# Performance work log

Hardware: AMD Instinct MI355X
Metric: run time of the kernel (lower is better)

The kernel has to match this reference:

```python
import jax, jax.numpy as jnp
import numpy as np

GAMMA = 2.0
SMOOTH = 1e-08
ALPHA_SMOOTH = 0.1


def setup_inputs() -> dict:
    key = jax.random.key(0)
    k1, k2 = jax.random.split(key)
    N, C, H, W = 8, 16, 512, 512
    logits = jax.random.normal(k1, (N, C, H, W), dtype=jnp.float32)
    target = jax.random.randint(k2, (N, H, W), 0, C, dtype=jnp.int64)
    return {"logits": logits, "target": target}


def _adaptive_alpha(target, num_classes):
    # histogram of class counts (fixed size -> jit friendly)
    counts = jnp.zeros((num_classes,), jnp.float32).at[target.reshape(-1)].add(1.0)
    total = jnp.asarray(target.size, jnp.float32)
    freq = counts / total
    w = 1.0 / (freq + ALPHA_SMOOTH)
    present = counts > 0
    wsum = jnp.sum(jnp.where(present, w, 0.0))
    # absent classes keep alpha = 1.0, matching torch.unique-based assignment
    return jnp.where(present, w / wsum, 1.0)


def reference(logits, target):
    # logits: (N, C, H, W) float; target: (N, H, W) int
    C = logits.shape[1]
    alpha = _adaptive_alpha(target, C)  # (C,)
    p = jax.nn.softmax(logits, axis=1)
    # gather probability of true class: equivalent to the one-hot loop, since
    # focal_c is multiplied by t_c so only positions with target==c contribute,
    # where p_t == p_c.
    p_true = jnp.take_along_axis(p, target[:, None, :, :], axis=1)[:, 0]  # (N,H,W)
    focal = alpha[target] * (1.0 - p_true + SMOOTH) ** GAMMA * (-jnp.log(p_true + SMOOTH))
    num_positives = jnp.asarray(target.size, jnp.float32)  # one-hot sum
    return jnp.sum(focal) / (num_positives + SMOOTH)
```

## Files before the change

### kernel.cpp

```cpp
#include <hip/hip_runtime.h>

#define HWSZ   262144
#define NCLS   16
#define NPIX   2097152
#define NQ     524288
#define GRID   1024
#define BLOCK  256
#define NCOPY  16

__global__ __launch_bounds__(BLOCK) void focal_main(
    const float* __restrict__ logits,
    const int*   __restrict__ target,
    float*       __restrict__ pb,
    unsigned*    __restrict__ pc)
{
    __shared__ float    sbin[NCOPY][NCLS];
    __shared__ unsigned scnt[NCOPY][NCLS];
    for (int i = threadIdx.x; i < NCOPY * NCLS; i += BLOCK) {
        ((float*)sbin)[i]    = 0.0f;
        ((unsigned*)scnt)[i] = 0u;
    }
    __syncthreads();

    const int copy = threadIdx.x & (NCOPY - 1);

    for (int q = blockIdx.x * BLOCK + threadIdx.x; q < NQ; q += GRID * BLOCK) {
        const int n  = q >> 16;
        const int s4 = (q & 65535) << 2;
        const float* base = logits + (size_t)n * (NCLS * HWSZ) + s4;
        const int4 t4 = *(const int4*)(target + ((size_t)q << 2));

        float4 ssum = make_float4(0.f, 0.f, 0.f, 0.f);
        float4 et   = make_float4(0.f, 0.f, 0.f, 0.f);
#pragma unroll
        for (int c = 0; c < NCLS; ++c) {
            const float4 v = *(const float4*)(base + (size_t)c * HWSZ);
            float ex;
            ex = __expf(v.x); ssum.x += ex; et.x = (t4.x == c) ? ex : et.x;
            ex = __expf(v.y); ssum.y += ex; et.y = (t4.y == c) ? ex : et.y;
            ex = __expf(v.z); ssum.z += ex; et.z = (t4.z == c) ? ex : et.z;
            ex = __expf(v.w); ssum.w += ex; et.w = (t4.w == c) ? ex : et.w;
        }

        float p, b;
        p = et.x * __builtin_amdgcn_rcpf(ssum.x);
        b = 1.0f - p + 1e-8f; b = b * b * (-__logf(p + 1e-8f));
        atomicAdd(&sbin[copy][t4.x & 15], b);
        atomicAdd(&scnt[copy][t4.x & 15], 1u);

        p = et.y * __builtin_amdgcn_rcpf(ssum.y);
        b = 1.0f - p + 1e-8f; b = b * b * (-__logf(p + 1e-8f));
        atomicAdd(&sbin[copy][t4.y & 15], b);
        atomicAdd(&scnt[copy][t4.y & 15], 1u);

        p = et.z * __builtin_amdgcn_rcpf(ssum.z);
        b = 1.0f - p + 1e-8f; b = b * b * (-__logf(p + 1e-8f));
        atomicAdd(&sbin[copy][t4.z & 15], b);
        atomicAdd(&scnt[copy][t4.z & 15], 1u);

        p = et.w * __builtin_amdgcn_rcpf(ssum.w);
        b = 1.0f - p + 1e-8f; b = b * b * (-__logf(p + 1e-8f));
        atomicAdd(&sbin[copy][t4.w & 15], b);
        atomicAdd(&scnt[copy][t4.w & 15], 1u);
    }
    __syncthreads();

    if (threadIdx.x < NCLS) {
        float    s  = 0.0f;
        unsigned n2 = 0u;
        for (int k = 0; k < NCOPY; ++k) {
            s  += sbin[k][threadIdx.x];
            n2 += scnt[k][threadIdx.x];
        }
        pb[threadIdx.x * GRID + blockIdx.x] = s;
        pc[threadIdx.x * GRID + blockIdx.x] = n2;
    }
}

__global__ __launch_bounds__(256) void focal_finalize(
    const float*    __restrict__ pb,
    const unsigned* __restrict__ pc,
    float*          __restrict__ out)
{
    __shared__ double   sb[NCLS][16];
    __shared__ unsigned sn[NCLS][16];
    const int c   = threadIdx.x >> 4;
    const int seg = threadIdx.x & 15;

    const float4* pbv = (const float4*)(pb + c * GRID + seg * 64);
    const uint4*  pcv = (const uint4*)(pc + c * GRID + seg * 64);
    double   s = 0.0;
    unsigned n = 0u;
#pragma unroll
    for (int i = 0; i < 16; ++i) {
        const float4 f = pbv[i];
        s += (double)f.x + (double)f.y + (double)f.z + (double)f.w;
        const uint4 u = pcv[i];
        n += u.x + u.y + u.z + u.w;
    }
    sb[c][seg] = s;
    sn[c][seg] = n;
    __syncthreads();

    if (threadIdx.x < NCLS) {
        double   S   = 0.0;
        unsigned cnt = 0u;
        for (int k = 0; k < 16; ++k) { S += sb[threadIdx.x][k]; cnt += sn[threadIdx.x][k]; }
        sb[threadIdx.x][0] = S;
        sn[threadIdx.x][0] = cnt;
    }
    __syncthreads();

    if (threadIdx.x == 0) {
        const double total = (double)NPIX;
        double w[NCLS];
        double wsum = 0.0;
        for (int k = 0; k < NCLS; ++k) {
            const double freq = (double)sn[k][0] / total;
            w[k] = 1.0 / (freq + 0.1);
            if (sn[k][0] > 0u) wsum += w[k];
        }
        double loss = 0.0;
        for (int k = 0; k < NCLS; ++k) {
            const double alpha = (sn[k][0] > 0u) ? (w[k] / wsum) : 1.0;
            loss += alpha * sb[k][0];
        }
        out[0] = (float)(loss / (total + 1e-8));
    }
}

extern "C" void kernel_launch(void* const* d_in, const int* in_sizes, int n_in,
                              void* d_out, int out_size, void* d_ws, size_t ws_size,
                              hipStream_t stream)
{
    const float* logits = (const float*)d_in[0];
    const int*   target = (const int*)d_in[1];

    float*    pb = (float*)d_ws;
    unsigned* pc = (unsigned*)((char*)d_ws + (size_t)NCLS * GRID * sizeof(float));

    focal_main<<<GRID, BLOCK, 0, stream>>>(logits, target, pb, pc);
    focal_finalize<<<1, 256, 0, stream>>>(pb, pc, (float*)d_out);
}
```

Baseline: 200.5 us.

## Use one quad per thread, nontemporal loads, and fixed-point global atomics

Doubles the grid so each thread handles exactly one 4-pixel quad with no grid-stride loop, and switches the logits and target loads to nontemporal loads. Per-block class sums are turned into 64-bit fixed-point integers and atomically added to global accumulators, which keeps the result deterministic. That removes the per-block partial-sum arrays and lets the finalize kernel shrink to a single thread. The cost is an extra memset launch plus global atomic contention from 2048 blocks on 16 addresses. Fixed-point rounding also adds some quantization error.

After: 209.4 us. 1.04x slower.

```diff
diff --git a/kernel.cpp b/kernel.cpp
--- a/kernel.cpp
+++ b/kernel.cpp
@@ -4,15 +4,19 @@
 #define NCLS   16
 #define NPIX   2097152
 #define NQ     524288
-#define GRID   1024
+#define GRID   2048
 #define BLOCK  256
 #define NCOPY  16
+#define FP_SCALE 16777216.0
+
+typedef float fx4 __attribute__((ext_vector_type(4)));
+typedef int   ix4 __attribute__((ext_vector_type(4)));
 
 __global__ __launch_bounds__(BLOCK) void focal_main(
     const float* __restrict__ logits,
     const int*   __restrict__ target,
-    float*       __restrict__ pb,
-    unsigned*    __restrict__ pc)
+    unsigned long long* __restrict__ acc_s,
+    unsigned*           __restrict__ acc_n)
 {
     __shared__ float    sbin[NCOPY][NCLS];
     __shared__ unsigned scnt[NCOPY][NCLS];
@@ -23,46 +27,46 @@
     __syncthreads();
 
     const int copy = threadIdx.x & (NCOPY - 1);
+    const int q    = blockIdx.x * BLOCK + threadIdx.x;
+    const int n    = q >> 16;
+    const int s4   = (q & 65535) << 2;
+    const float* base = logits + (size_t)n * (NCLS * HWSZ) + s4;
 
-    for (int q = blockIdx.x * BLOCK + threadIdx.x; q < NQ; q += GRID * BLOCK) {
-        const int n  = q >> 16;
-        const int s4 = (q & 65535) << 2;
-        const float* base = logits + (size_t)n * (NCLS * HWSZ) + s4;
-        const int4 t4 = *(const int4*)(target + ((size_t)q << 2));
+    const ix4 t4 = __builtin_nontemporal_load((const ix4*)(target + ((size_t)q << 2)));
 
-        float4 ssum = make_float4(0.f, 0.f, 0.f, 0.f);
-        float4 et   = make_float4(0.f, 0.f, 0.f, 0.f);
+    fx4 ssum = (fx4){0.f, 0.f, 0.f, 0.f};
+    fx4 et   = (fx4){0.f, 0.f, 0.f, 0.f};
 #pragma unroll
-        for (int c = 0; c < NCLS; ++c) {
-            const float4 v = *(const float4*)(base + (size_t)c * HWSZ);
-            float ex;
-            ex = __expf(v.x); ssum.x += ex; et.x = (t4.x == c) ? ex : et.x;
-            ex = __expf(v.y); ssum.y += ex; et.y = (t4.y == c) ? ex : et.y;
-            ex = __expf(v.z); ssum.z += ex; et.z = (t4.z == c) ? ex : et.z;
-            ex = __expf(v.w); ssum.w += ex; et.w = (t4.w == c) ? ex : et.w;
-        }
+    for (int c = 0; c < NCLS; ++c) {
+        const fx4 v = __builtin_nontemporal_load((const fx4*)(base + (size_t)c * HWSZ));
+        float ex;
+        ex = __expf(v.x); ssum.x += ex; et.x = (t4.x == c) ? ex : et.x;
+        ex = __expf(v.y); ssum.y += ex; et.y = (t4.y == c) ? ex : et.y;
+        ex = __expf(v.z); ssum.z += ex; et.z = (t4.z == c) ? ex : et.z;
+        ex = __expf(v.w); ssum.w += ex; et.w = (t4.w == c) ? ex : et.w;
+    }
 
-        float p, b;
-        p = et.x * __builtin_amdgcn_rcpf(ssum.x);
-        b = 1.0f - p + 1e-8f; b = b * b * (-__logf(p + 1e-8f));
-        atomicAdd(&sbin[copy][t4.x & 15], b);
-        atomicAdd(&scnt[copy][t4.x & 15], 1u);
+    float p, b;
+    p = et.x * __builtin_amdgcn_rcpf(ssum.x);
+    b = 1.0f - p + 1e-8f; b = b * b * (-__logf(p + 1e-8f));
+    atomicAdd(&sbin[copy][t4.x & 15], b);
+    atomicAdd(&scnt[copy][t4.x & 15], 1u);
 
-        p = et.y * __builtin_amdgcn_rcpf(ssum.y);
-        b = 1.0f - p + 1e-8f; b = b * b * (-__logf(p + 1e-8f));
-        atomicAdd(&sbin[copy][t4.y & 15], b);
-        atomicAdd(&scnt[copy][t4.y & 15], 1u);
+    p = et.y * __builtin_amdgcn_rcpf(ssum.y);
+    b = 1.0f - p + 1e-8f; b = b * b * (-__logf(p + 1e-8f));
+    atomicAdd(&sbin[copy][t4.y & 15], b);
+    atomicAdd(&scnt[copy][t4.y & 15], 1u);
 
-        p = et.z * __builtin_amdgcn_rcpf(ssum.z);
-        b = 1.0f - p + 1e-8f; b = b * b * (-__logf(p + 1e-8f));
-        atomicAdd(&sbin[copy][t4.z & 15], b);
-        atomicAdd(&scnt[copy][t4.z & 15], 1u);
+    p = et.z * __builtin_amdgcn_rcpf(ssum.z);
+    b = 1.0f - p + 1e-8f; b = b * b * (-__logf(p + 1e-8f));
+    atomicAdd(&sbin[copy][t4.z & 15], b);
+    atomicAdd(&scnt[copy][t4.z & 15], 1u);
 
-        p = et.w * __builtin_amdgcn_rcpf(ssum.w);
-        b = 1.0f - p + 1e-8f; b = b * b * (-__logf(p + 1e-8f));
-        atomicAdd(&sbin[copy][t4.w & 15], b);
-        atomicAdd(&scnt[copy][t4.w & 15], 1u);
-    }
+    p = et.w * __builtin_amdgcn_rcpf(ssum.w);
+    b = 1.0f - p + 1e-8f; b = b * b * (-__logf(p + 1e-8f));
+    atomicAdd(&sbin[copy][t4.w & 15], b);
+    atomicAdd(&scnt[copy][t4.w & 15], 1u);
+
     __syncthreads();
 
     if (threadIdx.x < NCLS) {
@@ -72,58 +76,32 @@
             s  += sbin[k][threadIdx.x];
             n2 += scnt[k][threadIdx.x];
         }
-        pb[threadIdx.x * GRID + blockIdx.x] = s;
-        pc[threadIdx.x * GRID + blockIdx.x] = n2;
+        atomicAdd(&acc_s[threadIdx.x],
+                  (unsigned long long)((double)s * FP_SCALE + 0.5));
+        atomicAdd(&acc_n[threadIdx.x], n2);
     }
 }
 
-__global__ __launch_bounds__(256) void focal_finalize(
-    const float*    __restrict__ pb,
-    const unsigned* __restrict__ pc,
-    float*          __restrict__ out)
+__global__ __launch_bounds__(64) void focal_finalize(
+    const unsigned long long* __restrict__ acc_s,
+    const unsigned*           __restrict__ acc_n,
+    float*                    __restrict__ out)
 {
-    __shared__ double   sb[NCLS][16];
-    __shared__ unsigned sn[NCLS][16];
-    const int c   = threadIdx.x >> 4;
-    const int seg = threadIdx.x & 15;
-
-    const float4* pbv = (const float4*)(pb + c * GRID + seg * 64);
-    const uint4*  pcv = (const uint4*)(pc + c * GRID + seg * 64);
-    double   s = 0.0;
-    unsigned n = 0u;
-#pragma unroll
-    for (int i = 0; i < 16; ++i) {
-        const float4 f = pbv[i];
-        s += (double)f.x + (double)f.y + (double)f.z + (double)f.w;
-        const uint4 u = pcv[i];
-        n += u.x + u.y + u.z + u.w;
-    }
-    sb[c][seg] = s;
-    sn[c][seg] = n;
-    __syncthreads();
-
-    if (threadIdx.x < NCLS) {
-        double   S   = 0.0;
-        unsigned cnt = 0u;
-        for (int k = 0; k < 16; ++k) { S += sb[threadIdx.x][k]; cnt += sn[threadIdx.x][k]; }
-        sb[threadIdx.x][0] = S;
-        sn[threadIdx.x][0] = cnt;
-    }
-    __syncthreads();
-
     if (threadIdx.x == 0) {
         const double total = (double)NPIX;
         double w[NCLS];
         double wsum = 0.0;
+        unsigned cnt[NCLS];
         for (int k = 0; k < NCLS; ++k) {
-            const double freq = (double)sn[k][0] / total;
+            cnt[k] = acc_n[k];
+            const double freq = (double)cnt[k] / total;
             w[k] = 1.0 / (freq + 0.1);
-            if (sn[k][0] > 0u) wsum += w[k];
+            if (cnt[k] > 0u) wsum += w[k];
         }
         double loss = 0.0;
         for (int k = 0; k < NCLS; ++k) {
-            const double alpha = (sn[k][0] > 0u) ? (w[k] / wsum) : 1.0;
-            loss += alpha * sb[k][0];
+            const double alpha = (cnt[k] > 0u) ? (w[k] / wsum) : 1.0;
+            loss += alpha * ((double)acc_s[k] * (1.0 / FP_SCALE));
         }
         out[0] = (float)(loss / (total + 1e-8));
     }
@@ -136,9 +114,10 @@
     const float* logits = (const float*)d_in[0];
     const int*   target = (const int*)d_in[1];
 
-    float*    pb = (float*)d_ws;
-    unsigned* pc = (unsigned*)((char*)d_ws + (size_t)NCLS * GRID * sizeof(float));
+    unsigned long long* acc_s = (unsigned long long*)d_ws;
+    unsigned*           acc_n = (unsigned*)((char*)d_ws + 128);
 
-    focal_main<<<GRID, BLOCK, 0, stream>>>(logits, target, pb, pc);
-    focal_finalize<<<1, 256, 0, stream>>>(pb, pc, (float*)d_out);
+    (void)hipMemsetAsync(d_ws, 0, 256, stream);
+    focal_main<<<GRID, BLOCK, 0, stream>>>(logits, target, acc_s, acc_n);
+    focal_finalize<<<1, 64, 0, stream>>>(acc_s, acc_n, (float*)d_out);
 }
```
